# Kernel tuning notes

Measured on AMD Instinct MI355X. Metric: run time of the kernel, lower is better.

The kernel has to match this reference:

```python
import jax, jax.numpy as jnp
import numpy as np

METAPATH = [0, 1, 2]
NUM_REL = 5
N_NODES = 50000
N_EDGES = 800000
IN_DIM = 96
HID_DIM = 96
OUT_DIM = 96
LL_DIM = 64


def setup_inputs() -> dict:
    key = jax.random.key(0)
    ks = jax.random.split(key, 12)
    x = jax.random.normal(ks[0], (N_NODES, IN_DIM), dtype=jnp.float32)
    edge_index = jax.random.randint(ks[1], (2, N_EDGES), 0, N_NODES, dtype=jnp.int64)
    edge_type = jax.random.randint(ks[2], (N_EDGES,), 0, NUM_REL, dtype=jnp.int64)
    s1 = 1.0 / np.sqrt(IN_DIM)
    s2 = 1.0 / np.sqrt(HID_DIM)
    s3 = 1.0 / np.sqrt(OUT_DIM)
    w1 = jax.random.normal(ks[3], (NUM_REL, IN_DIM, HID_DIM), dtype=jnp.float32) * s1
    root1 = jax.random.normal(ks[4], (IN_DIM, HID_DIM), dtype=jnp.float32) * s1
    b1 = jnp.zeros((HID_DIM,), dtype=jnp.float32)
    w2 = jax.random.normal(ks[5], (NUM_REL, HID_DIM, OUT_DIM), dtype=jnp.float32) * s2
    root2 = jax.random.normal(ks[6], (HID_DIM, OUT_DIM), dtype=jnp.float32) * s2
    b2 = jnp.zeros((OUT_DIM,), dtype=jnp.float32)
    lin_w = jax.random.normal(ks[7], (OUT_DIM, LL_DIM), dtype=jnp.float32) * s3
    lin_b = jnp.zeros((LL_DIM,), dtype=jnp.float32)
    return {"x": x, "edge_index": edge_index, "edge_type": edge_type,
            "w1": w1, "root1": root1, "b1": b1,
            "w2": w2, "root2": root2, "b2": b2,
            "lin_w": lin_w, "lin_b": lin_b}


def _rgcn_layer(rel, h, edge_index, edge_type, W, root, bias):
    # flow='target_to_source': message from dst node, aggregated at src node.
    src, dst = edge_index[0], edge_index[1]
    mask = (edge_type == rel)
    msg = h[dst] @ W[rel]                      # [E, out] gather + per-relation GEMM
    msg = jnp.where(mask[:, None], msg, 0.0)
    agg = jax.ops.segment_sum(msg, src, num_segments=h.shape[0])   # scatter-add
    cnt = jax.ops.segment_sum(mask.astype(h.dtype), src, num_segments=h.shape[0])
    agg = agg / jnp.clip(cnt, 1.0)[:, None]    # mean normalization per target
    return agg + h @ root + bias


def reference(x, edge_index, edge_type, w1, root1, b1, w2, root2, b2, lin_w, lin_b):
    h = x
    for layer_index, rel in enumerate(METAPATH):
        if layer_index == 0:
            h = jax.nn.relu(_rgcn_layer(rel, h, edge_index, edge_type, w1, root1, b1))
        else:
            h = jax.nn.relu(_rgcn_layer(rel, h, edge_index, edge_type, w2, root2, b2))
    return h @ lin_w + lin_b
```

## Files before the change

### kernel.cpp

```cpp
#include <hip/hip_runtime.h>

#define NNODES 50000
#define NEDGES 800000
#define DIM 96
#define LLDIM 64
#define NRELS 3
#define SCAN_N (NRELS * NNODES)

#define BT_PLANE 18432
#define BT_LAYER (2 * BT_PLANE)
#define BTL_PLANE 6144
#define BT_LIN_OFF (3 * BT_LAYER)

typedef __attribute__((ext_vector_type(8))) short bf16x8;
typedef __attribute__((ext_vector_type(4))) float f32x4;

__device__ __forceinline__ unsigned short f2bf(float x) {
    union { float f; unsigned u; } v; v.f = x;
    unsigned r = v.u + 0x7fffu + ((v.u >> 16) & 1u);
    return (unsigned short)(r >> 16);
}
__device__ __forceinline__ float bf2f(unsigned short b) {
    union { unsigned u; float f; } v; v.u = ((unsigned)b) << 16;
    return v.f;
}


__global__ void hist_kernel(const int* __restrict__ ei, const int* __restrict__ et,
                            int* __restrict__ deg) {
    int e = blockIdx.x * 256 + threadIdx.x;
    if (e >= NEDGES) return;
    int r = et[e];
    if (r < NRELS) atomicAdd(&deg[r * NNODES + ei[e]], 1);
}

__global__ void scan1_kernel(const int* __restrict__ in, int* __restrict__ out,
                             int* __restrict__ partials, int n) {
    __shared__ int sdata[256];
    int tid = threadIdx.x;
    int base = blockIdx.x * 1024 + tid * 4;
    int v0 = (base + 0 < n) ? in[base + 0] : 0;
    int v1 = (base + 1 < n) ? in[base + 1] : 0;
    int v2 = (base + 2 < n) ? in[base + 2] : 0;
    int v3 = (base + 3 < n) ? in[base + 3] : 0;
    int tsum = v0 + v1 + v2 + v3;
    sdata[tid] = tsum;
    __syncthreads();
    for (int off = 1; off < 256; off <<= 1) {
        int x = sdata[tid];
        int y = (tid >= off) ? sdata[tid - off] : 0;
        __syncthreads();
        sdata[tid] = x + y;
        __syncthreads();
    }
    int excl = sdata[tid] - tsum;
    if (tid == 255) partials[blockIdx.x] = sdata[255];
    if (base + 0 < n) out[base + 0] = excl;
    excl += v0;
    if (base + 1 < n) out[base + 1] = excl;
    excl += v1;
    if (base + 2 < n) out[base + 2] = excl;
    excl += v2;
    if (base + 3 < n) out[base + 3] = excl;
}

__global__ void scan2_kernel(int* __restrict__ partials, int nb) {
    __shared__ int sdata[256];
    int tid = threadIdx.x;
    int v = (tid < nb) ? partials[tid] : 0;
    sdata[tid] = v;
    __syncthreads();
    for (int off = 1; off < 256; off <<= 1) {
        int x = sdata[tid];
        int y = (tid >= off) ? sdata[tid - off] : 0;
        __syncthreads();
        sdata[tid] = x + y;
        __syncthreads();
    }
    partials[tid] = sdata[tid] - v;
}

__global__ void scan3_kernel(int* __restrict__ out, int* __restrict__ cursor,
                             const int* __restrict__ partials, int n) {
    int idx = blockIdx.x * 256 + threadIdx.x;
    if (idx < n) {
        int v = out[idx] + partials[idx >> 10];
        out[idx] = v;
        cursor[idx] = v;
    }
}

__global__ void fill_kernel(const int* __restrict__ ei, const int* __restrict__ et,
                            int* __restrict__ cursor, int* __restrict__ col) {
    int e = blockIdx.x * 256 + threadIdx.x;
    if (e >= NEDGES) return;
    int r = et[e];
    if (r < NRELS) {
        int pos = atomicAdd(&cursor[r * NNODES + ei[e]], 1);
        col[pos] = ei[NEDGES + e];
    }
}


__global__ void prep_kernel(const float* __restrict__ w1, const float* __restrict__ root1,
                            const float* __restrict__ w2, const float* __restrict__ root2,
                            const float* __restrict__ lin_w,
                            unsigned short* __restrict__ bt, int* __restrict__ deg) {
    int idx = blockIdx.x * 256 + threadIdx.x;
    if (idx < SCAN_N) deg[idx] = 0;
    const int LYR = 96 * 192;
    if (idx < 3 * LYR) {
        int l = idx / LYR;
        int rem = idx % LYR;
        int c = rem / 192;
        int k = rem % 192;
        const float* Wm;
        const float* Rm;
        if (l == 0) { Wm = w1; Rm = root1; }
        else        { Wm = w2 + (size_t)l * 96 * 96; Rm = root2; }
        float v = (k < 96) ? Wm[(size_t)k * 96 + c] : Rm[(size_t)(k - 96) * 96 + c];
        unsigned short hi = f2bf(v);
        unsigned short lo = f2bf(v - bf2f(hi));
        int ph = k / 96, kk = k % 96;
        int ks = kk / 32, g = (kk & 31) >> 3, kr = k & 7;
        int cg = c >> 4, r = c & 15;
        size_t off = (((size_t)((ph * 3 + ks) * 6 + cg)) * 64 + g * 16 + r) * 8 + kr;
        unsigned short* base = bt + (size_t)l * BT_LAYER;
        base[off] = hi;
        base[BT_PLANE + off] = lo;
    } else if (idx < 3 * LYR + 64 * 96) {
        int rem = idx - 3 * LYR;
        int c = rem / 96;
        int k = rem % 96;
        float v = lin_w[(size_t)k * 64 + c];
        unsigned short hi = f2bf(v);
        unsigned short lo = f2bf(v - bf2f(hi));
        int ks = k / 32, g = (k & 31) >> 3, kr = k & 7;
        int cg = c >> 4, r = c & 15;
        size_t off = (((size_t)(ks * 4 + cg)) * 64 + g * 16 + r) * 8 + kr;
        unsigned short* base = bt + BT_LIN_OFF;
        base[off] = hi;
        base[BTL_PLANE + off] = lo;
    }
}


__device__ __forceinline__ void gather_to_lds(
    const float* __restrict__ h, const int* __restrict__ rs, const int* __restrict__ re,
    const int* __restrict__ col, int n0, int tid,
    unsigned short* Ah, unsigned short* Al) {
    const int nd = tid >> 2;
    const int node = n0 + nd;
    const int cq4 = (tid & 3) * 24;
    float a[24];
#pragma unroll
    for (int j = 0; j < 24; ++j) a[j] = 0.0f;
    int s = 0, e = 0;
    if (node < NNODES) { s = rs[node]; e = re[node]; }
    for (int i = s; i < e; ++i) {
        int d = col[i];
        const float* p = h + (size_t)d * DIM + cq4;
#pragma unroll
        for (int j6 = 0; j6 < 6; ++j6) {
            float4 v = *(const float4*)(p + j6 * 4);
            a[j6 * 4 + 0] += v.x; a[j6 * 4 + 1] += v.y;
            a[j6 * 4 + 2] += v.z; a[j6 * 4 + 3] += v.w;
        }
    }
    float scl = 1.0f / fmaxf((float)(e - s), 1.0f);
    int arow = nd * 104 + cq4;
#pragma unroll
    for (int jp = 0; jp < 12; ++jp) {
        float v0 = a[jp * 2] * scl, v1 = a[jp * 2 + 1] * scl;
        unsigned short h0 = f2bf(v0), h1 = f2bf(v1);
        unsigned short l0 = f2bf(v0 - bf2f(h0)), l1 = f2bf(v1 - bf2f(h1));
        *(unsigned int*)&Ah[arow + jp * 2] = (unsigned)h0 | ((unsigned)h1 << 16);
        *(unsigned int*)&Al[arow + jp * 2] = (unsigned)l0 | ((unsigned)l1 << 16);
    }
}

__device__ __forceinline__ void stage_h_to_lds(
    const float* __restrict__ src, int n0, int tid,
    unsigned short* Ah, unsigned short* Al) {
#pragma unroll
    for (int j = 0; j < 6; ++j) {
        int idx = tid + j * 256;
        int nd = idx / 24;
        int kq = idx % 24;
        int node = n0 + nd;
        if (node >= NNODES) node = NNODES - 1;
        float4 v = *(const float4*)(src + (size_t)node * DIM + kq * 4);
        unsigned short h0 = f2bf(v.x), h1 = f2bf(v.y), h2 = f2bf(v.z), h3 = f2bf(v.w);
        *(ushort4*)&Ah[nd * 104 + kq * 4] = make_ushort4(h0, h1, h2, h3);
        unsigned short l0 = f2bf(v.x - bf2f(h0));
        unsigned short l1 = f2bf(v.y - bf2f(h1));
        unsigned short l2 = f2bf(v.z - bf2f(h2));
        unsigned short l3 = f2bf(v.w - bf2f(h3));
        *(ushort4*)&Al[nd * 104 + kq * 4] = make_ushort4(l0, l1, l2, l3);
    }
}

#define KS_LOOP(PH)                                                                     \
    _Pragma("unroll")                                                                   \
    for (int ks = 0; ks < 3; ++ks) {                                                    \
        const int ko = ks * 32 + g * 8;                                                 \
        bf16x8 a0h = *(const bf16x8*)&Ah[(rb_base + r) * 104 + ko];                     \
        bf16x8 a1h = *(const bf16x8*)&Ah[(rb_base + 16 + r) * 104 + ko];                \
        bf16x8 a0l = *(const bf16x8*)&Al[(rb_base + r) * 104 + ko];                     \
        bf16x8 a1l = *(const bf16x8*)&Al[(rb_base + 16 + r) * 104 + ko];                \
        const unsigned short* bks = bt + ((size_t)(((PH) * 3 + ks) * 6) * 64 + lane) * 8;\
        _Pragma("unroll")                                                               \
        for (int ct = 0; ct < 3; ++ct) {                                                \
            const unsigned short* bp = bks + (size_t)(cg_base + ct) * 512;              \
            bf16x8 bhv = *(const bf16x8*)bp;                                            \
            bf16x8 blv = *(const bf16x8*)(bp + BT_PLANE);                               \
            acc[0][ct] = __builtin_amdgcn_mfma_f32_16x16x32_bf16(a0h, bhv, acc[0][ct], 0, 0, 0); \
            acc[1][ct] = __builtin_amdgcn_mfma_f32_16x16x32_bf16(a1h, bhv, acc[1][ct], 0, 0, 0); \
            acc[0][ct] = __builtin_amdgcn_mfma_f32_16x16x32_bf16(a0l, bhv, acc[0][ct], 0, 0, 0); \
            acc[1][ct] = __builtin_amdgcn_mfma_f32_16x16x32_bf16(a1l, bhv, acc[1][ct], 0, 0, 0); \
            acc[0][ct] = __builtin_amdgcn_mfma_f32_16x16x32_bf16(a0h, blv, acc[0][ct], 0, 0, 0); \
            acc[1][ct] = __builtin_amdgcn_mfma_f32_16x16x32_bf16(a1h, blv, acc[1][ct], 0, 0, 0); \
        }                                                                               \
    }

__global__ __launch_bounds__(256) void layer_fused_kernel(
    const float* __restrict__ h, const int* __restrict__ rs, const int* __restrict__ re,
    const int* __restrict__ col, const unsigned short* __restrict__ bt,
    const float* __restrict__ b, float* __restrict__ out) {
    __shared__ unsigned short Ah[64 * 104];
    __shared__ unsigned short Al[64 * 104];
    const int tid = threadIdx.x;
    const int lane = tid & 63;
    const int w = tid >> 6;
    const int r = lane & 15;
    const int g = lane >> 4;
    const int rb_base = (w >> 1) * 32;
    const int cg_base = (w & 1) * 3;
    const int n0 = blockIdx.x * 64;

    gather_to_lds(h, rs, re, col, n0, tid, Ah, Al);

    f32x4 acc[2][3];
#pragma unroll
    for (int i = 0; i < 2; ++i)
#pragma unroll
        for (int j = 0; j < 3; ++j) acc[i][j] = (f32x4){0.f, 0.f, 0.f, 0.f};

    __syncthreads();
    KS_LOOP(0)
    __syncthreads();
    stage_h_to_lds(h, n0, tid, Ah, Al);
    __syncthreads();
    KS_LOOP(1)

#pragma unroll
    for (int ct = 0; ct < 3; ++ct) {
        int colc = (cg_base + ct) * 16 + r;
        float bias = b[colc];
#pragma unroll
        for (int rbi = 0; rbi < 2; ++rbi) {
            int row0 = n0 + rb_base + rbi * 16 + g * 4;
#pragma unroll
            for (int j = 0; j < 4; ++j) {
                int node = row0 + j;
                if (node < NNODES)
                    out[(size_t)node * DIM + colc] = fmaxf(acc[rbi][ct][j] + bias, 0.0f);
            }
        }
    }
}


__global__ __launch_bounds__(256) void layer2_final_kernel(
    const float* __restrict__ h, const int* __restrict__ rs, const int* __restrict__ re,
    const int* __restrict__ col, const unsigned short* __restrict__ bt,
    const float* __restrict__ b, const unsigned short* __restrict__ btl,
    const float* __restrict__ LB, float* __restrict__ out) {
    __shared__ unsigned short Ah[64 * 104];
    __shared__ unsigned short Al[64 * 104];
    const int tid = threadIdx.x;
    const int lane = tid & 63;
    const int w = tid >> 6;
    const int r = lane & 15;
    const int g = lane >> 4;
    const int rb_base = (w >> 1) * 32;
    const int cg_base = (w & 1) * 3;
    const int n0 = blockIdx.x * 64;

    gather_to_lds(h, rs, re, col, n0, tid, Ah, Al);

    f32x4 acc[2][3];
#pragma unroll
    for (int i = 0; i < 2; ++i)
#pragma unroll
        for (int j = 0; j < 3; ++j) acc[i][j] = (f32x4){0.f, 0.f, 0.f, 0.f};

    __syncthreads();
    KS_LOOP(0)
    __syncthreads();
    stage_h_to_lds(h, n0, tid, Ah, Al);
    __syncthreads();
    KS_LOOP(1)

    __syncthreads();
#pragma unroll
    for (int ct = 0; ct < 3; ++ct) {
        int colc = (cg_base + ct) * 16 + r;
        float bias = b[colc];
#pragma unroll
        for (int rbi = 0; rbi < 2; ++rbi) {
            int row0 = rb_base + rbi * 16 + g * 4;
#pragma unroll
            for (int j = 0; j < 4; ++j) {
                float v = fmaxf(acc[rbi][ct][j] + bias, 0.0f);
                unsigned short hh = f2bf(v);
                unsigned short ll = f2bf(v - bf2f(hh));
                Ah[(row0 + j) * 104 + colc] = hh;
                Al[(row0 + j) * 104 + colc] = ll;
            }
        }
    }
    __syncthreads();

    const int cgf = (w & 1) * 2;
    f32x4 accf[2][2];
#pragma unroll
    for (int i = 0; i < 2; ++i)
#pragma unroll
        for (int j = 0; j < 2; ++j) accf[i][j] = (f32x4){0.f, 0.f, 0.f, 0.f};

#pragma unroll
    for (int ks = 0; ks < 3; ++ks) {
        const int ko = ks * 32 + g * 8;
        bf16x8 a0h = *(const bf16x8*)&Ah[(rb_base + r) * 104 + ko];
        bf16x8 a1h = *(const bf16x8*)&Ah[(rb_base + 16 + r) * 104 + ko];
        bf16x8 a0l = *(const bf16x8*)&Al[(rb_base + r) * 104 + ko];
        bf16x8 a1l = *(const bf16x8*)&Al[(rb_base + 16 + r) * 104 + ko];
        const unsigned short* bks = btl + ((size_t)(ks * 4) * 64 + lane) * 8;
#pragma unroll
        for (int ct = 0; ct < 2; ++ct) {
            const unsigned short* bp = bks + (size_t)(cgf + ct) * 512;
            bf16x8 bhv = *(const bf16x8*)bp;
            bf16x8 blv = *(const bf16x8*)(bp + BTL_PLANE);
            accf[0][ct] = __builtin_amdgcn_mfma_f32_16x16x32_bf16(a0h, bhv, accf[0][ct], 0, 0, 0);
            accf[1][ct] = __builtin_amdgcn_mfma_f32_16x16x32_bf16(a1h, bhv, accf[1][ct], 0, 0, 0);
            accf[0][ct] = __builtin_amdgcn_mfma_f32_16x16x32_bf16(a0l, bhv, accf[0][ct], 0, 0, 0);
            accf[1][ct] = __builtin_amdgcn_mfma_f32_16x16x32_bf16(a1l, bhv, accf[1][ct], 0, 0, 0);
            accf[0][ct] = __builtin_amdgcn_mfma_f32_16x16x32_bf16(a0h, blv, accf[0][ct], 0, 0, 0);
            accf[1][ct] = __builtin_amdgcn_mfma_f32_16x16x32_bf16(a1h, blv, accf[1][ct], 0, 0, 0);
        }
    }

#pragma unroll
    for (int ct = 0; ct < 2; ++ct) {
        int colc = (cgf + ct) * 16 + r;
        float bias = LB[colc];
#pragma unroll
        for (int rbi = 0; rbi < 2; ++rbi) {
            int row0 = n0 + rb_base + rbi * 16 + g * 4;
#pragma unroll
            for (int j = 0; j < 4; ++j) {
                int node = row0 + j;
                if (node < NNODES)
                    out[(size_t)node * LLDIM + colc] = accf[rbi][ct][j] + bias;
            }
        }
    }
}

extern "C" void kernel_launch(void* const* d_in, const int* in_sizes, int n_in,
                              void* d_out, int out_size, void* d_ws, size_t ws_size,
                              hipStream_t stream) {
    const float* x     = (const float*)d_in[0];
    const int*   ei    = (const int*)d_in[1];
    const int*   et    = (const int*)d_in[2];
    const float* w1    = (const float*)d_in[3];
    const float* root1 = (const float*)d_in[4];
    const float* b1    = (const float*)d_in[5];
    const float* w2    = (const float*)d_in[6];
    const float* root2 = (const float*)d_in[7];
    const float* b2    = (const float*)d_in[8];
    const float* lin_w = (const float*)d_in[9];
    const float* lin_b = (const float*)d_in[10];

    float* bufA = (float*)d_ws;
    float* bufB = bufA + (size_t)NNODES * DIM;
    int* deg       = (int*)(bufB + (size_t)NNODES * DIM);
    int* row_start = deg + SCAN_N;
    int* row_end   = row_start + SCAN_N;
    int* col       = row_end + SCAN_N;
    int* partials  = col + NEDGES;
    unsigned short* bt = (unsigned short*)(partials + 256);

    const int edge_blocks = (NEDGES + 255) / 256;
    const int scan_blocks = (SCAN_N + 1023) / 1024;
    const int node_tiles  = (NNODES + 63) / 64;
    const int prep_blocks = (SCAN_N + 255) / 256;

    prep_kernel<<<prep_blocks, 256, 0, stream>>>(w1, root1, w2, root2, lin_w, bt, deg);

    hist_kernel<<<edge_blocks, 256, 0, stream>>>(ei, et, deg);
    scan1_kernel<<<scan_blocks, 256, 0, stream>>>(deg, row_start, partials, SCAN_N);
    scan2_kernel<<<1, 256, 0, stream>>>(partials, scan_blocks);
    scan3_kernel<<<(SCAN_N + 255) / 256, 256, 0, stream>>>(row_start, row_end, partials, SCAN_N);
    fill_kernel<<<edge_blocks, 256, 0, stream>>>(ei, et, row_end, col);

    layer_fused_kernel<<<node_tiles, 256, 0, stream>>>(
        x, row_start + 0 * NNODES, row_end + 0 * NNODES, col,
        bt + 0 * (size_t)BT_LAYER, b1, bufA);

    layer_fused_kernel<<<node_tiles, 256, 0, stream>>>(
        bufA, row_start + 1 * NNODES, row_end + 1 * NNODES, col,
        bt + 1 * (size_t)BT_LAYER, b2, bufB);

    layer2_final_kernel<<<node_tiles, 256, 0, stream>>>(
        bufB, row_start + 2 * NNODES, row_end + 2 * NNODES, col,
        bt + 2 * (size_t)BT_LAYER, b2, bt + BT_LIN_OFF, lin_b, (float*)d_out);
}
```

Before: 221.3 us.

## Fuse three-pass scan into single-pass decoupled lookback and unroll gather by two

Replaces the three-kernel exclusive scan (block scan, partials scan, add-back) with one kernel. It takes a dynamic block ticket and does a decoupled lookback over per-block flags, which removes two launches and one full pass over the offset arrays. Separately, the CSR neighbour gather loop now processes two edges per iteration with two accumulator sets, so more independent loads are in flight. The cost is spin-waiting on flags, which relies on forward progress between blocks, and extra registers in the gather.

```diff
diff --git a/kernel.cpp b/kernel.cpp
--- a/kernel.cpp
+++ b/kernel.cpp
@@ -6,11 +6,13 @@
 #define LLDIM 64
 #define NRELS 3
 #define SCAN_N (NRELS * NNODES)
+#define SCAN_BLOCKS ((SCAN_N + 1023) / 1024)
 
 #define BT_PLANE 18432
 #define BT_LAYER (2 * BT_PLANE)
 #define BTL_PLANE 6144
 #define BT_LIN_OFF (3 * BT_LAYER)
+#define BT_TOTAL (3 * BT_LAYER + 2 * BTL_PLANE)
 
 typedef __attribute__((ext_vector_type(8))) short bf16x8;
 typedef __attribute__((ext_vector_type(4))) float f32x4;
@@ -34,11 +36,18 @@
     if (r < NRELS) atomicAdd(&deg[r * NNODES + ei[e]], 1);
 }
 
-__global__ void scan1_kernel(const int* __restrict__ in, int* __restrict__ out,
-                             int* __restrict__ partials, int n) {
+__global__ void scan_fused_kernel(const int* __restrict__ in, int* __restrict__ out,
+                                  int* __restrict__ cursor,
+                                  unsigned long long* __restrict__ flags,
+                                  int* __restrict__ ticket, int n) {
     __shared__ int sdata[256];
+    __shared__ int sbid;
+    __shared__ int sprefix;
     int tid = threadIdx.x;
-    int base = blockIdx.x * 1024 + tid * 4;
+    if (tid == 0) sbid = atomicAdd(ticket, 1);
+    __syncthreads();
+    int bid = sbid;
+    int base = bid * 1024 + tid * 4;
     int v0 = (base + 0 < n) ? in[base + 0] : 0;
     int v1 = (base + 1 < n) ? in[base + 1] : 0;
     int v2 = (base + 2 < n) ? in[base + 2] : 0;
@@ -54,40 +63,28 @@
         __syncthreads();
     }
     int excl = sdata[tid] - tsum;
-    if (tid == 255) partials[blockIdx.x] = sdata[255];
-    if (base + 0 < n) out[base + 0] = excl;
+    if (tid == 0) {
+        int T = sdata[255];
+        atomicExch(&flags[bid], ((unsigned long long)(unsigned)T << 32) | 1ULL);
+        int prefix = 0;
+        for (int j = bid - 1; j >= 0; --j) {
+            unsigned long long f;
+            do { f = atomicAdd(&flags[j], 0ULL); } while ((f & 3ULL) == 0ULL);
+            prefix += (int)(f >> 32);
+            if ((f & 3ULL) == 2ULL) break;
+        }
+        atomicExch(&flags[bid], ((unsigned long long)(unsigned)(prefix + T) << 32) | 2ULL);
+        sprefix = prefix;
+    }
+    __syncthreads();
+    excl += sprefix;
+    if (base + 0 < n) { out[base + 0] = excl; cursor[base + 0] = excl; }
     excl += v0;
-    if (base + 1 < n) out[base + 1] = excl;
+    if (base + 1 < n) { out[base + 1] = excl; cursor[base + 1] = excl; }
     excl += v1;
-    if (base + 2 < n) out[base + 2] = excl;
+    if (base + 2 < n) { out[base + 2] = excl; cursor[base + 2] = excl; }
     excl += v2;
-    if (base + 3 < n) out[base + 3] = excl;
-}
-
-__global__ void scan2_kernel(int* __restrict__ partials, int nb) {
-    __shared__ int sdata[256];
-    int tid = threadIdx.x;
-    int v = (tid < nb) ? partials[tid] : 0;
-    sdata[tid] = v;
-    __syncthreads();
-    for (int off = 1; off < 256; off <<= 1) {
-        int x = sdata[tid];
-        int y = (tid >= off) ? sdata[tid - off] : 0;
-        __syncthreads();
-        sdata[tid] = x + y;
-        __syncthreads();
-    }
-    partials[tid] = sdata[tid] - v;
-}
-
-__global__ void scan3_kernel(int* __restrict__ out, int* __restrict__ cursor,
-                             const int* __restrict__ partials, int n) {
-    int idx = blockIdx.x * 256 + threadIdx.x;
-    if (idx < n) {
-        int v = out[idx] + partials[idx >> 10];
-        out[idx] = v;
-        cursor[idx] = v;
-    }
+    if (base + 3 < n) { out[base + 3] = excl; cursor[base + 3] = excl; }
 }
 
 __global__ void fill_kernel(const int* __restrict__ ei, const int* __restrict__ et,
@@ -105,9 +102,12 @@
 __global__ void prep_kernel(const float* __restrict__ w1, const float* __restrict__ root1,
                             const float* __restrict__ w2, const float* __restrict__ root2,
                             const float* __restrict__ lin_w,
-                            unsigned short* __restrict__ bt, int* __restrict__ deg) {
+                            unsigned short* __restrict__ bt, int* __restrict__ deg,
+                            unsigned long long* __restrict__ flags, int* __restrict__ ticket) {
     int idx = blockIdx.x * 256 + threadIdx.x;
     if (idx < SCAN_N) deg[idx] = 0;
+    if (idx < 256) flags[idx] = 0ULL;
+    if (idx == 300) *ticket = 0;
     const int LYR = 96 * 192;
     if (idx < 3 * LYR) {
         int l = idx / LYR;
@@ -152,21 +152,39 @@
     const int nd = tid >> 2;
     const int node = n0 + nd;
     const int cq4 = (tid & 3) * 24;
-    float a[24];
-#pragma unroll
-    for (int j = 0; j < 24; ++j) a[j] = 0.0f;
+    float a[24], c2[24];
+#pragma unroll
+    for (int j = 0; j < 24; ++j) { a[j] = 0.0f; c2[j] = 0.0f; }
     int s = 0, e = 0;
     if (node < NNODES) { s = rs[node]; e = re[node]; }
-    for (int i = s; i < e; ++i) {
+    int i = s;
+    for (; i + 2 <= e; i += 2) {
+        int d0 = col[i];
+        int d1 = col[i + 1];
+        const float* p0 = h + (size_t)d0 * DIM + cq4;
+        const float* p1 = h + (size_t)d1 * DIM + cq4;
+#pragma unroll
+        for (int j6 = 0; j6 < 6; ++j6) {
+            float4 u = *(const float4*)(p0 + j6 * 4);
+            float4 v = *(const float4*)(p1 + j6 * 4);
+            a[j6 * 4 + 0] += u.x; a[j6 * 4 + 1] += u.y;
+            a[j6 * 4 + 2] += u.z; a[j6 * 4 + 3] += u.w;
+            c2[j6 * 4 + 0] += v.x; c2[j6 * 4 + 1] += v.y;
+            c2[j6 * 4 + 2] += v.z; c2[j6 * 4 + 3] += v.w;
+        }
+    }
+    if (i < e) {
         int d = col[i];
         const float* p = h + (size_t)d * DIM + cq4;
 #pragma unroll
         for (int j6 = 0; j6 < 6; ++j6) {
-            float4 v = *(const float4*)(p + j6 * 4);
-            a[j6 * 4 + 0] += v.x; a[j6 * 4 + 1] += v.y;
-            a[j6 * 4 + 2] += v.z; a[j6 * 4 + 3] += v.w;
-        }
-    }
+            float4 u = *(const float4*)(p + j6 * 4);
+            a[j6 * 4 + 0] += u.x; a[j6 * 4 + 1] += u.y;
+            a[j6 * 4 + 2] += u.z; a[j6 * 4 + 3] += u.w;
+        }
+    }
+#pragma unroll
+    for (int j = 0; j < 24; ++j) a[j] += c2[j];
     float scl = 1.0f / fmaxf((float)(e - s), 1.0f);
     int arow = nd * 104 + cq4;
 #pragma unroll
@@ -391,18 +409,19 @@
     int* col       = row_end + SCAN_N;
     int* partials  = col + NEDGES;
     unsigned short* bt = (unsigned short*)(partials + 256);
+    unsigned long long* flags = (unsigned long long*)(bt + BT_TOTAL);
+    int* ticket = (int*)(flags + 256);
 
     const int edge_blocks = (NEDGES + 255) / 256;
-    const int scan_blocks = (SCAN_N + 1023) / 1024;
     const int node_tiles  = (NNODES + 63) / 64;
     const int prep_blocks = (SCAN_N + 255) / 256;
 
-    prep_kernel<<<prep_blocks, 256, 0, stream>>>(w1, root1, w2, root2, lin_w, bt, deg);
+    prep_kernel<<<prep_blocks, 256, 0, stream>>>(w1, root1, w2, root2, lin_w, bt, deg,
+                                                 flags, ticket);
 
     hist_kernel<<<edge_blocks, 256, 0, stream>>>(ei, et, deg);
-    scan1_kernel<<<scan_blocks, 256, 0, stream>>>(deg, row_start, partials, SCAN_N);
-    scan2_kernel<<<1, 256, 0, stream>>>(partials, scan_blocks);
-    scan3_kernel<<<(SCAN_N + 255) / 256, 256, 0, stream>>>(row_start, row_end, partials, SCAN_N);
+    scan_fused_kernel<<<SCAN_BLOCKS, 256, 0, stream>>>(deg, row_start, row_end,
+                                                       flags, ticket, SCAN_N);
     fill_kernel<<<edge_blocks, 256, 0, stream>>>(ei, et, row_end, col);
 
     layer_fused_kernel<<<node_tiles, 256, 0, stream>>>(
```

After: 248.1 us. 1.12x slower.
